# Kernel optimization log

Hardware: AMD Instinct MI355X
Metric: run time of the kernel (lower is better)

The kernel has to match this reference:

```python
import jax, jax.numpy as jnp
import numpy as np

CONTEXT_LENGTH = 2048
D_MODEL = 1024
N_HEADS = 16
D_HEAD = 64
ROPE_BASE = 10000.0
STD = 0.02


def rope(x, sines, cosines):
    # x: [b, s, h, d]; sines/cosines: [s, d//2]; interleaved even/odd pairing
    x_even = x[..., ::2]
    x_odd = x[..., 1::2]
    c = cosines[None, :, None, :]
    s = sines[None, :, None, :]
    out_even = x_even * c - x_odd * s
    out_odd = x_even * s + x_odd * c
    return jnp.stack((out_even, out_odd), axis=-1).reshape(x.shape)


def setup_inputs() -> dict:
    key = jax.random.key(0)
    k1, k2, k3, k4, k5 = jax.random.split(key, 5)
    x = jax.random.normal(k1, (2, 2048, D_MODEL), dtype=jnp.float32)
    key_weight = STD * jax.random.normal(k2, (N_HEADS, D_HEAD, D_MODEL), dtype=jnp.float32)
    query_weight = STD * jax.random.normal(k3, (N_HEADS, D_HEAD, D_MODEL), dtype=jnp.float32)
    value_weight = STD * jax.random.normal(k4, (N_HEADS, D_HEAD, D_MODEL), dtype=jnp.float32)
    output_weight = STD * jax.random.normal(k5, (D_MODEL, N_HEADS, D_HEAD), dtype=jnp.float32)
    angles = ROPE_BASE ** (-2.0 * jnp.arange(D_HEAD // 2, dtype=jnp.float32) / D_HEAD)
    positions = jnp.arange(CONTEXT_LENGTH, dtype=jnp.float32)
    apos = positions[:, None] * angles[None, :]  # [context, d_head//2]
    sines = jnp.sin(apos)
    cosines = jnp.cos(apos)
    return {"x": x, "key_weight": key_weight, "query_weight": query_weight,
            "value_weight": value_weight, "output_weight": output_weight,
            "sines": sines, "cosines": cosines}


def reference(x, key_weight, query_weight, value_weight, output_weight, sines, cosines):
    s = x.shape[1]
    sn, cs = sines[:s], cosines[:s]
    keys = jnp.einsum('hdm,bpm->bphd', key_weight, x)
    queries = jnp.einsum('hdm,bpm->bphd', query_weight, x)
    values = jnp.einsum('hdm,bpm->bphd', value_weight, x)
    keys = rope(keys, sn, cs)
    queries = rope(queries, sn, cs)
    # NOTE: no 1/sqrt(d_head) scaling, faithful to source
    scores = jnp.einsum('bkhd,bqhd->bhqk', keys, queries)
    mask = jnp.tril(jnp.ones((s, s), dtype=bool))  # causal (task='next_token')
    scores = jnp.where(mask[None, None], scores, -jnp.inf)
    pattern = jax.nn.softmax(scores, axis=-1)
    outputs = jnp.einsum('bhqk,bkhd->bqhd', pattern, values)
    return jnp.einsum('mhd,bphd->bpm', output_weight, outputs)
```

## Files before the change

kernel.cpp:

```cpp
#include <hip/hip_runtime.h>
#include <hip/hip_bf16.h>
#include <stdint.h>

typedef __bf16 bf16_t;
typedef bf16_t bf16x4 __attribute__((ext_vector_type(4)));
typedef bf16_t bf16x8 __attribute__((ext_vector_type(8)));
typedef float  f32x4  __attribute__((ext_vector_type(4)));

#define GAS __attribute__((address_space(1)))
#define LAS __attribute__((address_space(3)))

__device__ inline void gld_lds16(const void* g, void* l) {
    __builtin_amdgcn_global_load_lds((const GAS void*)g, (LAS void*)l, 16, 0, 0);
}

__device__ inline int swz(int row, int colbyte) {
    return row * 128 + (colbyte ^ ((row & 7) << 4));
}

__global__ __launch_bounds__(256) void k_cvt5(const float* __restrict__ i0, bf16_t* __restrict__ o0,
                                              const float* __restrict__ i1, bf16_t* __restrict__ o1,
                                              const float* __restrict__ i2, bf16_t* __restrict__ o2,
                                              const float* __restrict__ i3, bf16_t* __restrict__ o3,
                                              const float* __restrict__ i4, bf16_t* __restrict__ o4) {
    const float* in; bf16_t* out; int n;
    switch (blockIdx.y) {
        case 0: in = i0; out = o0; n = 4194304; break;
        case 1: in = i1; out = o1; n = 1048576; break;
        case 2: in = i2; out = o2; n = 1048576; break;
        case 3: in = i3; out = o3; n = 1048576; break;
        default: in = i4; out = o4; n = 1048576; break;
    }
    int i = (blockIdx.x * 256 + threadIdx.x) * 8;
    if (i >= n) return;
    f32x4 v0 = *(const f32x4*)(in + i);
    f32x4 v1 = *(const f32x4*)(in + i + 4);
    bf16x8 o;
    o[0] = (bf16_t)v0[0]; o[1] = (bf16_t)v0[1]; o[2] = (bf16_t)v0[2]; o[3] = (bf16_t)v0[3];
    o[4] = (bf16_t)v1[0]; o[5] = (bf16_t)v1[1]; o[6] = (bf16_t)v1[2]; o[7] = (bf16_t)v1[3];
    *(bf16x8*)(out + i) = o;
}

__global__ __launch_bounds__(256) void k_rope(bf16_t* __restrict__ Q, bf16_t* __restrict__ Kt,
                                              const float* __restrict__ sn,
                                              const float* __restrict__ cs) {
    int idx = blockIdx.x * 256 + threadIdx.x;
    bf16_t* T = blockIdx.y ? Kt : Q;
    int row = idx >> 9;
    int pi  = idx & 511;
    int h = pi >> 5, i = pi & 31;
    int p = row & 2047;
    float c = cs[p * 32 + i], s = sn[p * 32 + i];
    bf16_t* ptr = T + (size_t)row * 1024 + h * 64 + 2 * i;
    float e = (float)ptr[0], o = (float)ptr[1];
    ptr[0] = (bf16_t)(e * c - o * s);
    ptr[1] = (bf16_t)(e * s + o * c);
}

template <typename OutT>
__global__ __launch_bounds__(256) void k_gemm_bt(
    const bf16_t* __restrict__ A,
    const bf16_t* __restrict__ B0, const bf16_t* __restrict__ B1,
    OutT* __restrict__ C0, OutT* __restrict__ C1,
    int M, int N, int K) {
    const bf16_t* B = blockIdx.z == 0 ? B0 : B1;
    OutT*         C = blockIdx.z == 0 ? C0 : C1;
    const int BK = 32;
    __shared__ bf16_t As[128 * BK];
    __shared__ bf16_t Bs[128 * BK];
    int tid = threadIdx.x;
    int lane = tid & 63, wid = tid >> 6;
    int row0 = blockIdx.y * 128, col0 = blockIdx.x * 128;
    int wr = (wid >> 1) * 64, wc = (wid & 1) * 64;
    int lr = lane & 15, kg = lane >> 4;

    f32x4 acc[4][4];
#pragma unroll
    for (int i = 0; i < 4; ++i)
#pragma unroll
        for (int j = 0; j < 4; ++j) acc[i][j] = (f32x4){0.f, 0.f, 0.f, 0.f};

    int ob = tid * 16;
    for (int k0 = 0; k0 < K; k0 += BK) {
        __syncthreads();
#pragma unroll
        for (int p = 0; p < 2; ++p) {
            int off = p * 4096 + ob;
            int r = off >> 6;
            int cb = off & 63;
            gld_lds16((const char*)A + ((size_t)(row0 + r) * K + k0) * 2 + cb, (char*)As + off);
            gld_lds16((const char*)B + ((size_t)(col0 + r) * K + k0) * 2 + cb, (char*)Bs + off);
        }
        __syncthreads();
        bf16x8 af[4], bfr[4];
#pragma unroll
        for (int mi = 0; mi < 4; ++mi)
            af[mi] = *(const bf16x8*)&As[(wr + mi * 16 + lr) * BK + kg * 8];
#pragma unroll
        for (int ni = 0; ni < 4; ++ni)
            bfr[ni] = *(const bf16x8*)&Bs[(wc + ni * 16 + lr) * BK + kg * 8];
#pragma unroll
        for (int mi = 0; mi < 4; ++mi)
#pragma unroll
            for (int ni = 0; ni < 4; ++ni)
                acc[mi][ni] = __builtin_amdgcn_mfma_f32_16x16x32_bf16(af[mi], bfr[ni],
                                                                      acc[mi][ni], 0, 0, 0);
    }
#pragma unroll
    for (int mi = 0; mi < 4; ++mi)
#pragma unroll
        for (int ni = 0; ni < 4; ++ni)
#pragma unroll
            for (int r = 0; r < 4; ++r) {
                int row = row0 + wr + mi * 16 + kg * 4 + r;
                int col = col0 + wc + ni * 16 + lr;
                C[(size_t)row * N + col] = (OutT)acc[mi][ni][r];
            }
}

__global__ __launch_bounds__(256, 2) void k_flash(const bf16_t* __restrict__ Q,
                                                  const bf16_t* __restrict__ K,
                                                  const bf16_t* __restrict__ Vt,
                                                  bf16_t* __restrict__ Ob) {
    const int DM = 1024, S = 2048, NB = 4096;
    int h = blockIdx.y, b = blockIdx.z;
    int tid = threadIdx.x, lane = tid & 63, wid = tid >> 6;
    int lr = lane & 15, kg = lane >> 4;
    int rowbase = b * S;
    int colbase = h * 64;
    int quad = b ? (15 - (int)blockIdx.x) : (int)blockIdx.x;
    int s = quad * 4 + wid;
    int spos = s * 32;
    int kbmax = s >> 1;

    __shared__ bf16_t Ps[4][32 * 64];
    char* Pw = (char*)&Ps[wid][0];

    const bf16_t* Kg = K + (size_t)rowbase * DM + colbase;
    const bf16_t* Vg = Vt + (size_t)colbase * NB + rowbase;

#define LOADK(kb, dst)                                                               \
    _Pragma("unroll") for (int ni = 0; ni < 4; ++ni)                                 \
    _Pragma("unroll") for (int s2 = 0; s2 < 2; ++s2)                                 \
        dst[ni * 2 + s2] =                                                           \
            *(const bf16x8*)&Kg[(size_t)((kb) * 64 + ni * 16 + lr) * DM + s2 * 32 + kg * 8];

#define LOADV(kb, dst)                                                               \
    _Pragma("unroll") for (int nd = 0; nd < 4; ++nd)                                 \
    _Pragma("unroll") for (int s2 = 0; s2 < 2; ++s2)                                 \
        dst[nd * 2 + s2] =                                                           \
            *(const bf16x8*)&Vg[(size_t)(nd * 16 + lr) * NB + (kb) * 64 + s2 * 32 + kg * 8];

    bf16x8 qf[2][2];
#pragma unroll
    for (int mi = 0; mi < 2; ++mi)
#pragma unroll
        for (int s2 = 0; s2 < 2; ++s2)
            qf[mi][s2] = *(const bf16x8*)&Q[(size_t)(rowbase + spos + mi * 16 + lr) * DM +
                                            colbase + s2 * 32 + kg * 8];

    f32x4 Oa[2][4];
    float m_run[2], l_run[2];
#pragma unroll
    for (int mi = 0; mi < 2; ++mi) {
        m_run[mi] = -1e30f;
        l_run[mi] = 0.f;
#pragma unroll
        for (int nd = 0; nd < 4; ++nd) Oa[mi][nd] = (f32x4){0.f, 0.f, 0.f, 0.f};
    }

    bf16x8 kf[8], vf[8];
    LOADK(0, kf);
    LOADV(0, vf);

#pragma unroll 1
    for (int kb = 0; kb <= kbmax; ++kb) {
        f32x4 sa[2][4];
#pragma unroll
        for (int mi = 0; mi < 2; ++mi)
#pragma unroll
            for (int ni = 0; ni < 4; ++ni) sa[mi][ni] = (f32x4){0.f, 0.f, 0.f, 0.f};
        __builtin_amdgcn_s_setprio(1);
#pragma unroll
        for (int s2 = 0; s2 < 2; ++s2)
#pragma unroll
            for (int ni = 0; ni < 4; ++ni)
#pragma unroll
                for (int mi = 0; mi < 2; ++mi)
                    sa[mi][ni] = __builtin_amdgcn_mfma_f32_16x16x32_bf16(
                        kf[ni * 2 + s2], qf[mi][s2], sa[mi][ni], 0, 0, 0);
        __builtin_amdgcn_s_setprio(0);

        bool pre = kb < kbmax;
        if (pre) { LOADK(kb + 1, kf); }

        if (kb == kbmax) {
#pragma unroll
            for (int mi = 0; mi < 2; ++mi) {
                int qpos = spos + mi * 16 + lr;
#pragma unroll
                for (int ni = 0; ni < 4; ++ni)
#pragma unroll
                    for (int r = 0; r < 4; ++r)
                        if (kb * 64 + ni * 16 + kg * 4 + r > qpos) sa[mi][ni][r] = -1e30f;
            }
        }

#pragma unroll
        for (int mi = 0; mi < 2; ++mi) {
            float mx = -1e30f;
#pragma unroll
            for (int ni = 0; ni < 4; ++ni)
                mx = fmaxf(mx, fmaxf(fmaxf(sa[mi][ni][0], sa[mi][ni][1]),
                                     fmaxf(sa[mi][ni][2], sa[mi][ni][3])));
            mx = fmaxf(mx, __shfl_xor(mx, 16));
            mx = fmaxf(mx, __shfl_xor(mx, 32));
            float mo = m_run[mi];
            float mn = fmaxf(mo, mx);
            float sc = __expf(mo - mn);
            m_run[mi] = mn;
            float rs = 0.f;
#pragma unroll
            for (int ni = 0; ni < 4; ++ni) {
                bf16x4 pk;
#pragma unroll
                for (int r = 0; r < 4; ++r) {
                    float pv = __expf(sa[mi][ni][r] - mn);
                    rs += pv;
                    pk[r] = (bf16_t)pv;
                }
                *(bf16x4*)(Pw + swz(mi * 16 + lr, (ni * 16 + kg * 4) * 2)) = pk;
            }
            rs += __shfl_xor(rs, 16);
            rs += __shfl_xor(rs, 32);
            l_run[mi] = l_run[mi] * sc + rs;
#pragma unroll
            for (int nd = 0; nd < 4; ++nd) {
                Oa[mi][nd][0] *= sc; Oa[mi][nd][1] *= sc;
                Oa[mi][nd][2] *= sc; Oa[mi][nd][3] *= sc;
            }
        }

#pragma unroll
        for (int mi = 0; mi < 2; ++mi) {
#pragma unroll
            for (int s2 = 0; s2 < 2; ++s2) {
                bf16x8 pf = *(const bf16x8*)(Pw + swz(mi * 16 + lr, s2 * 64 + kg * 16));
                __builtin_amdgcn_s_setprio(1);
#pragma unroll
                for (int nd = 0; nd < 4; ++nd)
                    Oa[mi][nd] = __builtin_amdgcn_mfma_f32_16x16x32_bf16(
                        vf[nd * 2 + s2], pf, Oa[mi][nd], 0, 0, 0);
                __builtin_amdgcn_s_setprio(0);
            }
        }

        if (pre) { LOADV(kb + 1, vf); }
    }

#pragma unroll
    for (int mi = 0; mi < 2; ++mi) {
        float inv = 1.f / l_run[mi];
        size_t row = (size_t)(rowbase + spos + mi * 16 + lr);
#pragma unroll
        for (int nd = 0; nd < 4; ++nd) {
            bf16x4 o;
#pragma unroll
            for (int r = 0; r < 4; ++r) o[r] = (bf16_t)(Oa[mi][nd][r] * inv);
            *(bf16x4*)&Ob[row * DM + colbase + nd * 16 + kg * 4] = o;
        }
    }
#undef LOADK
#undef LOADV
}

extern "C" void kernel_launch(void* const* d_in, const int* in_sizes, int n_in,
                              void* d_out, int out_size, void* d_ws, size_t ws_size,
                              hipStream_t stream) {
    const float* x  = (const float*)d_in[0];
    const float* wk = (const float*)d_in[1];
    const float* wq = (const float*)d_in[2];
    const float* wv = (const float*)d_in[3];
    const float* wo = (const float*)d_in[4];
    const float* sn = (const float*)d_in[5];
    const float* cs = (const float*)d_in[6];
    float* out = (float*)d_out;
    (void)in_sizes; (void)n_in; (void)out_size; (void)ws_size;

    char* ws = (char*)d_ws;
    const size_t MB = 1024 * 1024;
    bf16_t* xb  = (bf16_t*)(ws + 0);
    bf16_t* wqb = (bf16_t*)(ws + 8 * MB);
    bf16_t* wkb = (bf16_t*)(ws + 10 * MB);
    bf16_t* wvb = (bf16_t*)(ws + 12 * MB);
    bf16_t* wob = (bf16_t*)(ws + 14 * MB);
    bf16_t* Qb  = (bf16_t*)(ws + 16 * MB);
    bf16_t* Kb  = (bf16_t*)(ws + 24 * MB);
    bf16_t* Vtb = (bf16_t*)(ws + 32 * MB);
    bf16_t* Ob  = (bf16_t*)(ws + 40 * MB);

    k_cvt5<<<dim3(2048, 5), 256, 0, stream>>>(x, xb, wq, wqb, wk, wkb, wv, wvb, wo, wob);

    k_gemm_bt<bf16_t><<<dim3(8, 32, 2), 256, 0, stream>>>(
        xb, wqb, wkb, Qb, Kb, 4096, 1024, 1024);
    k_gemm_bt<bf16_t><<<dim3(32, 8, 1), 256, 0, stream>>>(
        wvb, xb, xb, Vtb, Vtb, 1024, 4096, 1024);

    k_rope<<<dim3(8192, 2), 256, 0, stream>>>(Qb, Kb, sn, cs);

    k_flash<<<dim3(16, 16, 2), 256, 0, stream>>>(Qb, Kb, Vtb, Ob);

    k_gemm_bt<float><<<dim3(8, 32, 1), 256, 0, stream>>>(
        Ob, wob, wob, out, out, 4096, 1024, 1024);
}
```

Measured before the change: 165.6 us.

## Switch flash attention to 32x32x16 MFMA tiles with per-lane query rows

Rewrites the flash-attention inner loop so it uses 32x32x16 bf16 MFMA instructions instead of 16x16x32. Each lane now owns a single query row across 32 key columns, which changes the operand load layouts, the masking indices and the P staging layout in LDS. This halves the number of MFMA issues and shortens the softmax reductions to one cross-half shuffle per step. In exchange, the larger accumulator tiles raise register pressure under the two-blocks-per-SM launch bound.

```diff
diff --git a/kernel.cpp b/kernel.cpp
--- a/kernel.cpp
+++ b/kernel.cpp
@@ -6,6 +6,7 @@
 typedef bf16_t bf16x4 __attribute__((ext_vector_type(4)));
 typedef bf16_t bf16x8 __attribute__((ext_vector_type(8)));
 typedef float  f32x4  __attribute__((ext_vector_type(4)));
+typedef float  f32x16 __attribute__((ext_vector_type(16)));
 
 #define GAS __attribute__((address_space(1)))
 #define LAS __attribute__((address_space(3)))
@@ -125,13 +126,14 @@
     const int DM = 1024, S = 2048, NB = 4096;
     int h = blockIdx.y, b = blockIdx.z;
     int tid = threadIdx.x, lane = tid & 63, wid = tid >> 6;
-    int lr = lane & 15, kg = lane >> 4;
+    int ql = lane & 31, hi = lane >> 5;
     int rowbase = b * S;
     int colbase = h * 64;
     int quad = b ? (15 - (int)blockIdx.x) : (int)blockIdx.x;
     int s = quad * 4 + wid;
     int spos = s * 32;
     int kbmax = s >> 1;
+    int q = spos + ql;
 
     __shared__ bf16_t Ps[4][32 * 64];
     char* Pw = (char*)&Ps[wid][0];
@@ -140,34 +142,29 @@
     const bf16_t* Vg = Vt + (size_t)colbase * NB + rowbase;
 
 #define LOADK(kb, dst)                                                               \
-    _Pragma("unroll") for (int ni = 0; ni < 4; ++ni)                                 \
-    _Pragma("unroll") for (int s2 = 0; s2 < 2; ++s2)                                 \
-        dst[ni * 2 + s2] =                                                           \
-            *(const bf16x8*)&Kg[(size_t)((kb) * 64 + ni * 16 + lr) * DM + s2 * 32 + kg * 8];
+    _Pragma("unroll") for (int t = 0; t < 2; ++t)                                    \
+    _Pragma("unroll") for (int c = 0; c < 4; ++c)                                    \
+        dst[t * 4 + c] = *(const bf16x8*)&Kg[(size_t)((kb) * 64 + t * 32 + ql) * DM  \
+                                             + c * 16 + hi * 8];
 
 #define LOADV(kb, dst)                                                               \
-    _Pragma("unroll") for (int nd = 0; nd < 4; ++nd)                                 \
-    _Pragma("unroll") for (int s2 = 0; s2 < 2; ++s2)                                 \
-        dst[nd * 2 + s2] =                                                           \
-            *(const bf16x8*)&Vg[(size_t)(nd * 16 + lr) * NB + (kb) * 64 + s2 * 32 + kg * 8];
-
-    bf16x8 qf[2][2];
-#pragma unroll
-    for (int mi = 0; mi < 2; ++mi)
-#pragma unroll
-        for (int s2 = 0; s2 < 2; ++s2)
-            qf[mi][s2] = *(const bf16x8*)&Q[(size_t)(rowbase + spos + mi * 16 + lr) * DM +
-                                            colbase + s2 * 32 + kg * 8];
-
-    f32x4 Oa[2][4];
-    float m_run[2], l_run[2];
-#pragma unroll
-    for (int mi = 0; mi < 2; ++mi) {
-        m_run[mi] = -1e30f;
-        l_run[mi] = 0.f;
-#pragma unroll
-        for (int nd = 0; nd < 4; ++nd) Oa[mi][nd] = (f32x4){0.f, 0.f, 0.f, 0.f};
-    }
+    _Pragma("unroll") for (int od = 0; od < 2; ++od)                                 \
+    _Pragma("unroll") for (int kc = 0; kc < 4; ++kc)                                 \
+        dst[od * 4 + kc] = *(const bf16x8*)&Vg[(size_t)(od * 32 + ql) * NB           \
+                                               + (kb) * 64 + kc * 16 + hi * 8];
+
+    bf16x8 qf[4];
+#pragma unroll
+    for (int c = 0; c < 4; ++c)
+        qf[c] = *(const bf16x8*)&Q[(size_t)(rowbase + spos + ql) * DM + colbase +
+                                   c * 16 + hi * 8];
+
+    f32x16 Oa[2];
+#pragma unroll
+    for (int od = 0; od < 2; ++od)
+#pragma unroll
+        for (int r = 0; r < 16; ++r) Oa[od][r] = 0.f;
+    float m_run = -1e30f, l_run = 0.f;
 
     bf16x8 kf[8], vf[8];
     LOADK(0, kf);
@@ -175,20 +172,18 @@
 
 #pragma unroll 1
     for (int kb = 0; kb <= kbmax; ++kb) {
-        f32x4 sa[2][4];
-#pragma unroll
-        for (int mi = 0; mi < 2; ++mi)
-#pragma unroll
-            for (int ni = 0; ni < 4; ++ni) sa[mi][ni] = (f32x4){0.f, 0.f, 0.f, 0.f};
+        f32x16 sa[2];
+#pragma unroll
+        for (int t = 0; t < 2; ++t)
+#pragma unroll
+            for (int r = 0; r < 16; ++r) sa[t][r] = 0.f;
         __builtin_amdgcn_s_setprio(1);
 #pragma unroll
-        for (int s2 = 0; s2 < 2; ++s2)
-#pragma unroll
-            for (int ni = 0; ni < 4; ++ni)
-#pragma unroll
-                for (int mi = 0; mi < 2; ++mi)
-                    sa[mi][ni] = __builtin_amdgcn_mfma_f32_16x16x32_bf16(
-                        kf[ni * 2 + s2], qf[mi][s2], sa[mi][ni], 0, 0, 0);
+        for (int t = 0; t < 2; ++t)
+#pragma unroll
+            for (int c = 0; c < 4; ++c)
+                sa[t] = __builtin_amdgcn_mfma_f32_32x32x16_bf16(kf[t * 4 + c], qf[c],
+                                                                sa[t], 0, 0, 0);
         __builtin_amdgcn_s_setprio(0);
 
         bool pre = kb < kbmax;
@@ -196,80 +191,75 @@
 
         if (kb == kbmax) {
 #pragma unroll
-            for (int mi = 0; mi < 2; ++mi) {
-                int qpos = spos + mi * 16 + lr;
-#pragma unroll
-                for (int ni = 0; ni < 4; ++ni)
-#pragma unroll
-                    for (int r = 0; r < 4; ++r)
-                        if (kb * 64 + ni * 16 + kg * 4 + r > qpos) sa[mi][ni][r] = -1e30f;
+            for (int t = 0; t < 2; ++t)
+#pragma unroll
+                for (int g = 0; g < 4; ++g)
+#pragma unroll
+                    for (int j = 0; j < 4; ++j)
+                        if (kb * 64 + t * 32 + g * 8 + 4 * hi + j > q)
+                            sa[t][g * 4 + j] = -1e30f;
+        }
+
+        float mx = -1e30f;
+#pragma unroll
+        for (int t = 0; t < 2; ++t)
+#pragma unroll
+            for (int r = 0; r < 16; ++r) mx = fmaxf(mx, sa[t][r]);
+        mx = fmaxf(mx, __shfl_xor(mx, 32));
+        float mn = fmaxf(m_run, mx);
+        float sc = __expf(m_run - mn);
+        m_run = mn;
+        float rs = 0.f;
+#pragma unroll
+        for (int t = 0; t < 2; ++t)
+#pragma unroll
+            for (int r = 0; r < 16; ++r) {
+                float pv = __expf(sa[t][r] - mn);
+                sa[t][r] = pv;
+                rs += pv;
             }
-        }
-
-#pragma unroll
-        for (int mi = 0; mi < 2; ++mi) {
-            float mx = -1e30f;
-#pragma unroll
-            for (int ni = 0; ni < 4; ++ni)
-                mx = fmaxf(mx, fmaxf(fmaxf(sa[mi][ni][0], sa[mi][ni][1]),
-                                     fmaxf(sa[mi][ni][2], sa[mi][ni][3])));
-            mx = fmaxf(mx, __shfl_xor(mx, 16));
-            mx = fmaxf(mx, __shfl_xor(mx, 32));
-            float mo = m_run[mi];
-            float mn = fmaxf(mo, mx);
-            float sc = __expf(mo - mn);
-            m_run[mi] = mn;
-            float rs = 0.f;
-#pragma unroll
-            for (int ni = 0; ni < 4; ++ni) {
+        rs += __shfl_xor(rs, 32);
+        l_run = l_run * sc + rs;
+#pragma unroll
+        for (int od = 0; od < 2; ++od)
+#pragma unroll
+            for (int r = 0; r < 16; ++r) Oa[od][r] *= sc;
+
+#pragma unroll
+        for (int t = 0; t < 2; ++t)
+#pragma unroll
+            for (int g = 0; g < 4; ++g) {
                 bf16x4 pk;
 #pragma unroll
-                for (int r = 0; r < 4; ++r) {
-                    float pv = __expf(sa[mi][ni][r] - mn);
-                    rs += pv;
-                    pk[r] = (bf16_t)pv;
-                }
-                *(bf16x4*)(Pw + swz(mi * 16 + lr, (ni * 16 + kg * 4) * 2)) = pk;
+                for (int j = 0; j < 4; ++j) pk[j] = (bf16_t)sa[t][g * 4 + j];
+                *(bf16x4*)(Pw + swz(ql, (t * 32 + g * 8 + 4 * hi) * 2)) = pk;
             }
-            rs += __shfl_xor(rs, 16);
-            rs += __shfl_xor(rs, 32);
-            l_run[mi] = l_run[mi] * sc + rs;
-#pragma unroll
-            for (int nd = 0; nd < 4; ++nd) {
-                Oa[mi][nd][0] *= sc; Oa[mi][nd][1] *= sc;
-                Oa[mi][nd][2] *= sc; Oa[mi][nd][3] *= sc;
-            }
-        }
-
-#pragma unroll
-        for (int mi = 0; mi < 2; ++mi) {
-#pragma unroll
-            for (int s2 = 0; s2 < 2; ++s2) {
-                bf16x8 pf = *(const bf16x8*)(Pw + swz(mi * 16 + lr, s2 * 64 + kg * 16));
-                __builtin_amdgcn_s_setprio(1);
-#pragma unroll
-                for (int nd = 0; nd < 4; ++nd)
-                    Oa[mi][nd] = __builtin_amdgcn_mfma_f32_16x16x32_bf16(
-                        vf[nd * 2 + s2], pf, Oa[mi][nd], 0, 0, 0);
-                __builtin_amdgcn_s_setprio(0);
-            }
+
+#pragma unroll
+        for (int kc = 0; kc < 4; ++kc) {
+            bf16x8 pf = *(const bf16x8*)(Pw + swz(ql, kc * 32 + hi * 16));
+            __builtin_amdgcn_s_setprio(1);
+#pragma unroll
+            for (int od = 0; od < 2; ++od)
+                Oa[od] = __builtin_amdgcn_mfma_f32_32x32x16_bf16(vf[od * 4 + kc], pf,
+                                                                 Oa[od], 0, 0, 0);
+            __builtin_amdgcn_s_setprio(0);
         }
 
         if (pre) { LOADV(kb + 1, vf); }
     }
 
-#pragma unroll
-    for (int mi = 0; mi < 2; ++mi) {
-        float inv = 1.f / l_run[mi];
-        size_t row = (size_t)(rowbase + spos + mi * 16 + lr);
-#pragma unroll
-        for (int nd = 0; nd < 4; ++nd) {
+    float inv = 1.f / l_run;
+    size_t row = (size_t)(rowbase + spos + ql);
+#pragma unroll
+    for (int od = 0; od < 2; ++od)
+#pragma unroll
+        for (int g = 0; g < 4; ++g) {
             bf16x4 o;
 #pragma unroll
-            for (int r = 0; r < 4; ++r) o[r] = (bf16_t)(Oa[mi][nd][r] * inv);
-            *(bf16x4*)&Ob[row * DM + colbase + nd * 16 + kg * 4] = o;
+            for (int j = 0; j < 4; ++j) o[j] = (bf16_t)(Oa[od][g * 4 + j] * inv);
+            *(bf16x4*)&Ob[row * DM + colbase + od * 32 + g * 8 + 4 * hi] = o;
         }
-    }
 #undef LOADK
 #undef LOADV
 }
```

Measured after the change: 166.6 us, median of 2. Within noise of the previous version (+0.6%).
